# Kernel tuning notes

Hardware: AMD Instinct MI355X
Metric: run time of the kernel (lower is better)

## Reference

```python
import jax, jax.numpy as jnp
import numpy as np

NUM_HEADS = 32
NUM_KV_HEADS = 8
HEAD_DIM = 128
ROPE_THETA = 10000.0


def rotate_half(x):
    x1, x2 = jnp.split(x, 2, axis=-1)
    return jnp.concatenate((-x2, x1), axis=-1)


def setup_inputs() -> dict:
    key = jax.random.key(0)
    ks = jax.random.split(key, 5)
    B, S, H = 1, 2048, 4096
    KV = NUM_KV_HEADS * HEAD_DIM
    return {
        "hidden_states": jax.random.normal(ks[0], (B, S, H), dtype=jnp.float32),
        "position_ids": jnp.arange(S, dtype=jnp.int64 if jax.config.jax_enable_x64 else jnp.int32)[None, :].repeat(B, axis=0),
        "Wq": jax.random.normal(ks[1], (H, H), dtype=jnp.float32) * 0.02,
        "Wk": jax.random.normal(ks[2], (KV, H), dtype=jnp.float32) * 0.02,
        "Wv": jax.random.normal(ks[3], (KV, H), dtype=jnp.float32) * 0.02,
        "Wo": jax.random.normal(ks[4], (H, H), dtype=jnp.float32) * 0.02,
    }


def reference(hidden_states, position_ids, Wq, Wk, Wv, Wo):
    B, S, H = hidden_states.shape
    nh, nkv, hd = NUM_HEADS, NUM_KV_HEADS, HEAD_DIM
    n_rep = nh // nkv

    # QKV projections (torch Linear: y = x @ W^T)
    q = jnp.einsum('bsh,oh->bso', hidden_states, Wq).reshape(B, S, nh, hd).transpose(0, 2, 1, 3)
    k = jnp.einsum('bsh,oh->bso', hidden_states, Wk).reshape(B, S, nkv, hd).transpose(0, 2, 1, 3)
    v = jnp.einsum('bsh,oh->bso', hidden_states, Wv).reshape(B, S, nkv, hd).transpose(0, 2, 1, 3)

    # RoPE: cos/sin [B, 1, S, hd]
    inv_freq = 1.0 / (ROPE_THETA ** (jnp.arange(0, hd, 2, dtype=jnp.float32) / hd))
    freqs = position_ids.astype(jnp.float32)[..., None] * inv_freq  # [B, S, hd/2]
    emb = jnp.concatenate((freqs, freqs), axis=-1)                  # [B, S, hd]
    cos = jnp.cos(emb)[:, None, :, :]
    sin = jnp.sin(emb)[:, None, :, :]
    q = q * cos + rotate_half(q) * sin
    k = k * cos + rotate_half(k) * sin

    # GQA repeat_kv: [B, nkv, S, hd] -> [B, nh, S, hd]
    k = jnp.repeat(k, n_rep, axis=1)
    v = jnp.repeat(v, n_rep, axis=1)

    # eager attention with causal mask, softmax in fp32
    scores = jnp.einsum('bhqd,bhkd->bhqk', q, k) / jnp.sqrt(jnp.float32(hd))
    causal = jnp.tril(jnp.ones((S, S), dtype=bool))
    scores = jnp.where(causal[None, None], scores, jnp.finfo(scores.dtype).min)
    probs = jax.nn.softmax(scores.astype(jnp.float32), axis=-1).astype(q.dtype)
    attn = jnp.einsum('bhqk,bhkd->bhqd', probs, v)

    out = attn.transpose(0, 2, 1, 3).reshape(B, S, nh * hd)
    return jnp.einsum('bso,ho->bsh', out, Wo)
```

## Files before the change

kernel.cpp:

```cpp
#include <hip/hip_runtime.h>

typedef __bf16 bf16x8 __attribute__((ext_vector_type(8)));
typedef float f32x4 __attribute__((ext_vector_type(4)));
typedef unsigned int u32x4 __attribute__((ext_vector_type(4)));
typedef unsigned short u16x4 __attribute__((ext_vector_type(4)));
typedef unsigned short ushort_t;

#define S_LEN 2048
#define HDIM  4096
#define KVDIM 1024
#define NHEAD 32
#define NKV   8

__device__ __forceinline__ unsigned short f2b(float x) {
    unsigned int u = __builtin_bit_cast(unsigned int, x);
    u = (u + 0x7FFFu + ((u >> 16) & 1u)) >> 16;
    return (unsigned short)u;
}
__device__ __forceinline__ float b2f(unsigned short b) {
    unsigned int u = ((unsigned int)b) << 16;
    return __builtin_bit_cast(float, u);
}

__device__ __forceinline__ void gl_lds16(const void* g, void* s) {
    __builtin_amdgcn_global_load_lds(
        (const __attribute__((address_space(1))) unsigned int*)g,
        (__attribute__((address_space(3))) unsigned int*)s, 16, 0, 0);
}

__global__ void cvt_kernel(const float* __restrict__ in, unsigned short* __restrict__ out, int n4) {
    int i = blockIdx.x * 256 + threadIdx.x;
    if (i >= n4) return;
    f32x4 v = ((const f32x4*)in)[i];
    u16x4 o;
    o.x = f2b(v.x); o.y = f2b(v.y); o.z = f2b(v.z); o.w = f2b(v.w);
    ((u16x4*)out)[i] = o;
}

template <int MODE>
__device__ __forceinline__ void gemm_body(const unsigned short* __restrict__ A,
                                          const unsigned short* __restrict__ B,
                                          void* __restrict__ Cv,
                                          int M, int N, int K, int m0, int n0,
                                          unsigned short (*As)[64], unsigned short (*Bs)[64]) {
    const int tid = threadIdx.x;
    const int w = tid >> 6, lane = tid & 63, quad = lane >> 4, l15 = lane & 15;
    const int wy = w >> 1, wx = w & 1;
    const int srowb = w * 32 + (lane >> 3);
    const int gchunk = (lane & 7) ^ (lane >> 3);
    const int lcol = (lane & 7) * 8;

    f32x4 acc[4][4] = {};

    for (int k0 = 0; k0 < K; k0 += 64) {
#pragma unroll
        for (int p = 0; p < 4; ++p) {
            int r = srowb + p * 8;
            gl_lds16(&A[(size_t)(m0 + r) * K + k0 + gchunk * 8], &As[r][lcol]);
            gl_lds16(&B[(size_t)(n0 + r) * K + k0 + gchunk * 8], &Bs[r][lcol]);
        }
        __syncthreads();
#pragma unroll
        for (int t = 0; t < 2; ++t) {
            bf16x8 af[4], bfr[4];
#pragma unroll
            for (int mb = 0; mb < 4; ++mb)
                af[mb] = *(const bf16x8*)&As[wy * 64 + mb * 16 + l15][(((t * 4 + quad) ^ (l15 & 7)) * 8)];
#pragma unroll
            for (int nb = 0; nb < 4; ++nb)
                bfr[nb] = *(const bf16x8*)&Bs[wx * 64 + nb * 16 + l15][(((t * 4 + quad) ^ (l15 & 7)) * 8)];
#pragma unroll
            for (int mb = 0; mb < 4; ++mb)
#pragma unroll
                for (int nb = 0; nb < 4; ++nb)
                    acc[mb][nb] = __builtin_amdgcn_mfma_f32_16x16x32_bf16(af[mb], bfr[nb], acc[mb][nb], 0, 0, 0);
        }
        __syncthreads();
    }
#pragma unroll
    for (int mb = 0; mb < 4; ++mb)
#pragma unroll
        for (int nb = 0; nb < 4; ++nb)
#pragma unroll
            for (int r = 0; r < 4; ++r) {
                int row = m0 + wy * 64 + mb * 16 + quad * 4 + r;
                int col = n0 + wx * 64 + nb * 16 + l15;
                float v = acc[mb][nb][r];
                if (MODE == 0)
                    ((unsigned short*)Cv)[(size_t)row * N + col] = f2b(v);
                else if (MODE == 1)
                    ((unsigned short*)Cv)[(size_t)col * M + row] = f2b(v);
                else
                    ((float*)Cv)[(size_t)row * N + col] = v;
            }
}

template <int MODE>
__global__ __launch_bounds__(256) void gemm_nt(const unsigned short* __restrict__ A,
                                               const unsigned short* __restrict__ B,
                                               void* __restrict__ Cv, int M, int N, int K) {
    __shared__ unsigned short As[128][64];
    __shared__ unsigned short Bs[128][64];
    gemm_body<MODE>(A, B, Cv, M, N, K, blockIdx.y * 128, blockIdx.x * 128, As, Bs);
}

__global__ __launch_bounds__(256) void gemm_kv(const unsigned short* __restrict__ A,
                                               const unsigned short* __restrict__ Bk,
                                               const unsigned short* __restrict__ Bv,
                                               void* __restrict__ Ck, void* __restrict__ Cvt,
                                               int M, int K) {
    __shared__ unsigned short As[128][64];
    __shared__ unsigned short Bs[128][64];
    if (blockIdx.x < 8)
        gemm_body<0>(A, Bk, Ck, M, KVDIM, K, blockIdx.y * 128, blockIdx.x * 128, As, Bs);
    else
        gemm_body<1>(A, Bv, Cvt, M, KVDIM, K, blockIdx.y * 128, (blockIdx.x - 8) * 128, As, Bs);
}

__global__ void rope_kernel(unsigned short* __restrict__ Q, unsigned short* __restrict__ Kc,
                            const int* __restrict__ pos_ids) {
    int tid = blockIdx.x * 256 + threadIdx.x;
    int j = tid & 63;
    int head = (tid >> 6) % (NHEAD + NKV);
    int s = tid / (64 * (NHEAD + NKV));
    float pos = (float)pos_ids[s];
    float inv = exp2f(-(float)j * 0.20762050593046f);
    float ang = pos * inv;
    float sn, cs;
    __sincosf(ang, &sn, &cs);
    unsigned short* p;
    if (head < NHEAD)
        p = Q + (size_t)s * HDIM + head * 128;
    else
        p = Kc + (size_t)s * KVDIM + (head - NHEAD) * 128;
    float x1 = b2f(p[j]), x2 = b2f(p[j + 64]);
    p[j] = f2b(x1 * cs - x2 * sn);
    p[j + 64] = f2b(x2 * cs + x1 * sn);
}

__global__ __launch_bounds__(256) void attn_fwd(const unsigned short* __restrict__ Q,
                                                const unsigned short* __restrict__ Kb,
                                                const unsigned short* __restrict__ Vt,
                                                unsigned short* __restrict__ O) {
    __shared__ unsigned short Ks[64][136];
    __shared__ unsigned short Vts[128][72];
    __shared__ unsigned short Ps[4][16][80];

    const int qblk = (gridDim.y - 1) - blockIdx.y;
    const int h = blockIdx.x, kvh = h >> 2;
    const int tid = threadIdx.x, w = tid >> 6, lane = tid & 63;
    const int quad = lane >> 4, l15 = lane & 15;
    const int qg = qblk * 64 + w * 16 + l15;

    bf16x8 aq[4];
#pragma unroll
    for (int t = 0; t < 4; ++t)
        aq[t] = *(const bf16x8*)&Q[(size_t)qg * HDIM + h * 128 + t * 32 + quad * 8];

    f32x4 o[8] = {};
    float m_s = -3.0e38f, l_s = 0.f;
    const float cexp = 0.08838834764831845f * 1.4426950408889634f;

    const int kr0 = tid >> 4, ksg = tid & 15;
    const int vr0 = tid >> 3, vsg = tid & 7;

    u32x4 kpre[4], vpre[4];
#pragma unroll
    for (int p = 0; p < 4; ++p) {
        kpre[p] = *(const u32x4*)&Kb[(size_t)(kr0 + p * 16) * KVDIM + kvh * 128 + ksg * 8];
        vpre[p] = *(const u32x4*)&Vt[(size_t)(kvh * 128 + vr0 + p * 32) * S_LEN + vsg * 8];
    }

    for (int kt = 0; kt <= qblk; ++kt) {
#pragma unroll
        for (int p = 0; p < 4; ++p) {
            *(u32x4*)&Ks[kr0 + p * 16][ksg * 8] = kpre[p];
            *(u32x4*)&Vts[vr0 + p * 32][vsg * 8] = vpre[p];
        }
        __syncthreads();
        if (kt < qblk) {
            const int k0n = kt * 64 + 64;
#pragma unroll
            for (int p = 0; p < 4; ++p) {
                kpre[p] = *(const u32x4*)&Kb[(size_t)(k0n + kr0 + p * 16) * KVDIM + kvh * 128 + ksg * 8];
                vpre[p] = *(const u32x4*)&Vt[(size_t)(kvh * 128 + vr0 + p * 32) * S_LEN + k0n + vsg * 8];
            }
        }

        f32x4 sc[4] = {};
#pragma unroll
        for (int t = 0; t < 4; ++t)
#pragma unroll
            for (int mb = 0; mb < 4; ++mb) {
                bf16x8 ak = *(const bf16x8*)&Ks[mb * 16 + l15][t * 32 + quad * 8];
                sc[mb] = __builtin_amdgcn_mfma_f32_16x16x32_bf16(ak, aq[t], sc[mb], 0, 0, 0);
            }

        float vv[16];
        if (kt == qblk) {
#pragma unroll
            for (int mb = 0; mb < 4; ++mb)
#pragma unroll
                for (int r = 0; r < 4; ++r) {
                    int kl = mb * 16 + quad * 4 + r;
                    vv[mb * 4 + r] = (kl <= w * 16 + l15) ? sc[mb][r] * cexp : -3.0e38f;
                }
        } else {
#pragma unroll
            for (int mb = 0; mb < 4; ++mb)
#pragma unroll
                for (int r = 0; r < 4; ++r)
                    vv[mb * 4 + r] = sc[mb][r] * cexp;
        }
        float mx = vv[0];
#pragma unroll
        for (int i = 1; i < 16; ++i) mx = fmaxf(mx, vv[i]);
        mx = fmaxf(mx, __shfl_xor(mx, 16, 64));
        mx = fmaxf(mx, __shfl_xor(mx, 32, 64));
        float mnew = fmaxf(m_s, mx);
        float alpha = exp2f(m_s - mnew);
        m_s = mnew;
        float sum = 0.f;
        unsigned short pb[16];
#pragma unroll
        for (int i = 0; i < 16; ++i) {
            float pp = exp2f(vv[i] - mnew);
            sum += pp;
            pb[i] = f2b(pp);
        }
        sum += __shfl_xor(sum, 16, 64);
        sum += __shfl_xor(sum, 32, 64);
        l_s = l_s * alpha + sum;
#pragma unroll
        for (int mb = 0; mb < 4; ++mb) {
            u16x4 pk = {pb[mb * 4 + 0], pb[mb * 4 + 1], pb[mb * 4 + 2], pb[mb * 4 + 3]};
            *(u16x4*)&Ps[w][l15][mb * 16 + quad * 4] = pk;
        }
        float a4[4];
#pragma unroll
        for (int r = 0; r < 4; ++r) a4[r] = __shfl(alpha, quad * 20 + r, 64);
#pragma unroll
        for (int db = 0; db < 8; ++db)
#pragma unroll
            for (int r = 0; r < 4; ++r) o[db][r] *= a4[r];

        bf16x8 pa[2];
#pragma unroll
        for (int t = 0; t < 2; ++t)
            pa[t] = *(const bf16x8*)&Ps[w][l15][t * 32 + quad * 8];
#pragma unroll
        for (int db = 0; db < 8; ++db)
#pragma unroll
            for (int t = 0; t < 2; ++t) {
                bf16x8 vb = *(const bf16x8*)&Vts[db * 16 + l15][t * 32 + quad * 8];
                o[db] = __builtin_amdgcn_mfma_f32_16x16x32_bf16(pa[t], vb, o[db], 0, 0, 0);
            }
        __syncthreads();
    }

    float linv[4];
#pragma unroll
    for (int r = 0; r < 4; ++r) linv[r] = 1.0f / __shfl(l_s, quad * 20 + r, 64);
    const int qrow_base = qblk * 64 + w * 16 + quad * 4;
#pragma unroll
    for (int db = 0; db < 8; ++db)
#pragma unroll
        for (int r = 0; r < 4; ++r) {
            int row = qrow_base + r;
            int col = h * 128 + db * 16 + l15;
            O[(size_t)row * HDIM + col] = f2b(o[db][r] * linv[r]);
        }
}

extern "C" void kernel_launch(void* const* d_in, const int* in_sizes, int n_in,
                              void* d_out, int out_size, void* d_ws, size_t ws_size,
                              hipStream_t stream) {
    const float* hid = (const float*)d_in[0];
    const int* pos   = (const int*)d_in[1];
    const float* Wq  = (const float*)d_in[2];
    const float* Wk  = (const float*)d_in[3];
    const float* Wv  = (const float*)d_in[4];
    const float* Wo  = (const float*)d_in[5];
    float* out = (float*)d_out;

    char* ws = (char*)d_ws;
    unsigned short* hb   = (unsigned short*)(ws);
    unsigned short* Wqb  = (unsigned short*)(ws + 16777216);
    unsigned short* Wkb  = (unsigned short*)(ws + 50331648);
    unsigned short* Wvb  = (unsigned short*)(ws + 58720256);
    unsigned short* Wob  = (unsigned short*)(ws + 67108864);
    unsigned short* Qw   = (unsigned short*)(ws + 100663296);
    unsigned short* Kw   = (unsigned short*)(ws + 117440512);
    unsigned short* Vtw  = Wqb;
    unsigned short* attw = hb;

    cvt_kernel<<<(S_LEN * HDIM / 4 + 255) / 256, 256, 0, stream>>>(hid, hb, S_LEN * HDIM / 4);
    cvt_kernel<<<(HDIM * HDIM / 4 + 255) / 256, 256, 0, stream>>>(Wq, Wqb, HDIM * HDIM / 4);
    cvt_kernel<<<(KVDIM * HDIM / 4 + 255) / 256, 256, 0, stream>>>(Wk, Wkb, KVDIM * HDIM / 4);
    cvt_kernel<<<(KVDIM * HDIM / 4 + 255) / 256, 256, 0, stream>>>(Wv, Wvb, KVDIM * HDIM / 4);
    cvt_kernel<<<(HDIM * HDIM / 4 + 255) / 256, 256, 0, stream>>>(Wo, Wob, HDIM * HDIM / 4);

    gemm_nt<0><<<dim3(HDIM / 128, S_LEN / 128), 256, 0, stream>>>(hb, Wqb, Qw, S_LEN, HDIM, HDIM);
    gemm_kv<<<dim3(16, S_LEN / 128), 256, 0, stream>>>(hb, Wkb, Wvb, Kw, Vtw, S_LEN, HDIM);

    rope_kernel<<<S_LEN * (NHEAD + NKV) * 64 / 256, 256, 0, stream>>>(Qw, Kw, pos);

    attn_fwd<<<dim3(NHEAD, S_LEN / 64), 256, 0, stream>>>(Qw, Kw, Vtw, attw);

    gemm_nt<2><<<dim3(HDIM / 128, S_LEN / 128), 256, 0, stream>>>(attw, Wob, out, S_LEN, HDIM, HDIM);
}
```

Measured before the change: 561.0 us.

## Merge conversions and QKV GEMMs, use 128-row attention tiles with swizzled LDS

The five fp32-to-bf16 conversion launches become one kernel, and the Q and KV projection GEMMs become a single launch with 48 column blocks. V-transpose moves to its own workspace slot so it no longer aliases Wqb. The attention kernel now processes 128 query rows per block, two 16-row sub-tiles per wave, which halves K/V reloads across query blocks. It also drops LDS padding in favour of an XOR swizzle, skips fully masked sub-tiles, and sets a three-blocks-per-CU occupancy hint. These changes target launch overhead, K/V memory traffic and LDS bank conflicts, but raise register pressure and halve the number of attention blocks.

```diff
diff --git a/kernel.cpp b/kernel.cpp
--- a/kernel.cpp
+++ b/kernel.cpp
@@ -4,7 +4,6 @@
 typedef float f32x4 __attribute__((ext_vector_type(4)));
 typedef unsigned int u32x4 __attribute__((ext_vector_type(4)));
 typedef unsigned short u16x4 __attribute__((ext_vector_type(4)));
-typedef unsigned short ushort_t;
 
 #define S_LEN 2048
 #define HDIM  4096
@@ -28,13 +27,23 @@
         (__attribute__((address_space(3))) unsigned int*)s, 16, 0, 0);
 }
 
-__global__ void cvt_kernel(const float* __restrict__ in, unsigned short* __restrict__ out, int n4) {
-    int i = blockIdx.x * 256 + threadIdx.x;
-    if (i >= n4) return;
-    f32x4 v = ((const f32x4*)in)[i];
+__global__ void cvt_all(const float* __restrict__ hid, const float* __restrict__ Wq,
+                        const float* __restrict__ Wk, const float* __restrict__ Wv,
+                        const float* __restrict__ Wo,
+                        unsigned short* __restrict__ hb, unsigned short* __restrict__ Wqb,
+                        unsigned short* __restrict__ Wkb, unsigned short* __restrict__ Wvb,
+                        unsigned short* __restrict__ Wob) {
+    int g = blockIdx.x * 256 + threadIdx.x;
+    const float* src; unsigned short* dst; int off;
+    if (g < 2097152)      { src = hid; dst = hb;  off = g; }
+    else if (g < 6291456) { src = Wq;  dst = Wqb; off = g - 2097152; }
+    else if (g < 7340032) { src = Wk;  dst = Wkb; off = g - 6291456; }
+    else if (g < 8388608) { src = Wv;  dst = Wvb; off = g - 7340032; }
+    else                  { src = Wo;  dst = Wob; off = g - 8388608; }
+    f32x4 v = ((const f32x4*)src)[off];
     u16x4 o;
     o.x = f2b(v.x); o.y = f2b(v.y); o.z = f2b(v.z); o.w = f2b(v.w);
-    ((u16x4*)out)[i] = o;
+    ((u16x4*)dst)[off] = o;
 }
 
 template <int MODE>
@@ -95,26 +104,29 @@
             }
 }
 
-template <int MODE>
-__global__ __launch_bounds__(256) void gemm_nt(const unsigned short* __restrict__ A,
-                                               const unsigned short* __restrict__ B,
-                                               void* __restrict__ Cv, int M, int N, int K) {
+__global__ __launch_bounds__(256) void gemm_qkv(const unsigned short* __restrict__ A,
+                                                const unsigned short* __restrict__ Bq,
+                                                const unsigned short* __restrict__ Bk,
+                                                const unsigned short* __restrict__ Bv,
+                                                void* __restrict__ Cq, void* __restrict__ Ck,
+                                                void* __restrict__ Cvt) {
     __shared__ unsigned short As[128][64];
     __shared__ unsigned short Bs[128][64];
-    gemm_body<MODE>(A, B, Cv, M, N, K, blockIdx.y * 128, blockIdx.x * 128, As, Bs);
-}
-
-__global__ __launch_bounds__(256) void gemm_kv(const unsigned short* __restrict__ A,
-                                               const unsigned short* __restrict__ Bk,
-                                               const unsigned short* __restrict__ Bv,
-                                               void* __restrict__ Ck, void* __restrict__ Cvt,
-                                               int M, int K) {
+    const int bx = blockIdx.x, m0 = blockIdx.y * 128;
+    if (bx < 32)
+        gemm_body<0>(A, Bq, Cq, S_LEN, HDIM, HDIM, m0, bx * 128, As, Bs);
+    else if (bx < 40)
+        gemm_body<0>(A, Bk, Ck, S_LEN, KVDIM, HDIM, m0, (bx - 32) * 128, As, Bs);
+    else
+        gemm_body<1>(A, Bv, Cvt, S_LEN, KVDIM, HDIM, m0, (bx - 40) * 128, As, Bs);
+}
+
+__global__ __launch_bounds__(256) void gemm_o(const unsigned short* __restrict__ A,
+                                              const unsigned short* __restrict__ B,
+                                              void* __restrict__ Cv) {
     __shared__ unsigned short As[128][64];
     __shared__ unsigned short Bs[128][64];
-    if (blockIdx.x < 8)
-        gemm_body<0>(A, Bk, Ck, M, KVDIM, K, blockIdx.y * 128, blockIdx.x * 128, As, Bs);
-    else
-        gemm_body<1>(A, Bv, Cvt, M, KVDIM, K, blockIdx.y * 128, (blockIdx.x - 8) * 128, As, Bs);
+    gemm_body<2>(A, B, Cv, S_LEN, HDIM, HDIM, blockIdx.y * 128, blockIdx.x * 128, As, Bs);
 }
 
 __global__ void rope_kernel(unsigned short* __restrict__ Q, unsigned short* __restrict__ Kc,
@@ -138,31 +150,34 @@
     p[j + 64] = f2b(x2 * cs + x1 * sn);
 }
 
-__global__ __launch_bounds__(256) void attn_fwd(const unsigned short* __restrict__ Q,
-                                                const unsigned short* __restrict__ Kb,
-                                                const unsigned short* __restrict__ Vt,
-                                                unsigned short* __restrict__ O) {
-    __shared__ unsigned short Ks[64][136];
-    __shared__ unsigned short Vts[128][72];
-    __shared__ unsigned short Ps[4][16][80];
-
-    const int qblk = (gridDim.y - 1) - blockIdx.y;
+__global__ __launch_bounds__(256, 3) void attn_fwd(const unsigned short* __restrict__ Q,
+                                                   const unsigned short* __restrict__ Kb,
+                                                   const unsigned short* __restrict__ Vt,
+                                                   unsigned short* __restrict__ O) {
+    __shared__ unsigned short Ks[64][128];
+    __shared__ unsigned short Vts[128][64];
+    __shared__ unsigned short Ps[4][2][16][80];
+
+    const int qb = (gridDim.y - 1) - blockIdx.y;
     const int h = blockIdx.x, kvh = h >> 2;
     const int tid = threadIdx.x, w = tid >> 6, lane = tid & 63;
     const int quad = lane >> 4, l15 = lane & 15;
-    const int qg = qblk * 64 + w * 16 + l15;
-
-    bf16x8 aq[4];
-#pragma unroll
-    for (int t = 0; t < 4; ++t)
-        aq[t] = *(const bf16x8*)&Q[(size_t)qg * HDIM + h * 128 + t * 32 + quad * 8];
-
-    f32x4 o[8] = {};
-    float m_s = -3.0e38f, l_s = 0.f;
+
+    bf16x8 aq[2][4];
+#pragma unroll
+    for (int u = 0; u < 2; ++u)
+#pragma unroll
+        for (int t = 0; t < 4; ++t)
+            aq[u][t] = *(const bf16x8*)&Q[(size_t)(qb * 128 + w * 32 + u * 16 + l15) * HDIM +
+                                          h * 128 + t * 32 + quad * 8];
+
+    f32x4 o[2][8] = {};
+    float m_s[2] = {-3.0e38f, -3.0e38f}, l_s[2] = {0.f, 0.f};
     const float cexp = 0.08838834764831845f * 1.4426950408889634f;
 
     const int kr0 = tid >> 4, ksg = tid & 15;
     const int vr0 = tid >> 3, vsg = tid & 7;
+    const int ktmax = 2 * qb + 1;
 
     u32x4 kpre[4], vpre[4];
 #pragma unroll
@@ -171,14 +186,16 @@
         vpre[p] = *(const u32x4*)&Vt[(size_t)(kvh * 128 + vr0 + p * 32) * S_LEN + vsg * 8];
     }
 
-    for (int kt = 0; kt <= qblk; ++kt) {
+    for (int kt = 0; kt <= ktmax; ++kt) {
 #pragma unroll
         for (int p = 0; p < 4; ++p) {
-            *(u32x4*)&Ks[kr0 + p * 16][ksg * 8] = kpre[p];
-            *(u32x4*)&Vts[vr0 + p * 32][vsg * 8] = vpre[p];
+            int rk = kr0 + p * 16;
+            *(u32x4*)&Ks[rk][(ksg ^ (rk & 7)) * 8] = kpre[p];
+            int rv = vr0 + p * 32;
+            *(u32x4*)&Vts[rv][(vsg ^ (rv & 7)) * 8] = vpre[p];
         }
         __syncthreads();
-        if (kt < qblk) {
+        if (kt < ktmax) {
             const int k0n = kt * 64 + 64;
 #pragma unroll
             for (int p = 0; p < 4; ++p) {
@@ -187,89 +204,91 @@
             }
         }
 
-        f32x4 sc[4] = {};
-#pragma unroll
-        for (int t = 0; t < 4; ++t)
+        const int k0 = kt * 64;
+#pragma unroll
+        for (int u = 0; u < 2; ++u) {
+            const int qmin = qb * 128 + w * 32 + u * 16;
+            if (k0 > qmin + 15) continue;
+
+            f32x4 sc[4] = {};
+#pragma unroll
+            for (int t = 0; t < 4; ++t)
+#pragma unroll
+                for (int mb = 0; mb < 4; ++mb) {
+                    bf16x8 ak = *(const bf16x8*)&Ks[mb * 16 + l15][((t * 4 + quad) ^ (l15 & 7)) * 8];
+                    sc[mb] = __builtin_amdgcn_mfma_f32_16x16x32_bf16(ak, aq[u][t], sc[mb], 0, 0, 0);
+                }
+
+            const bool need_mask = (k0 + 63 > qmin);
+            const int qg = qmin + l15;
+            float mx = -3.0e38f;
+#pragma unroll
+            for (int mb = 0; mb < 4; ++mb)
+#pragma unroll
+                for (int r = 0; r < 4; ++r) {
+                    float v = sc[mb][r] * cexp;
+                    if (need_mask && (k0 + mb * 16 + quad * 4 + r > qg)) v = -3.0e38f;
+                    mx = fmaxf(mx, v);
+                }
+            mx = fmaxf(mx, __shfl_xor(mx, 16, 64));
+            mx = fmaxf(mx, __shfl_xor(mx, 32, 64));
+            float mnew = fmaxf(m_s[u], mx);
+            float alpha = exp2f(m_s[u] - mnew);
+            m_s[u] = mnew;
+            float sum = 0.f;
 #pragma unroll
             for (int mb = 0; mb < 4; ++mb) {
-                bf16x8 ak = *(const bf16x8*)&Ks[mb * 16 + l15][t * 32 + quad * 8];
-                sc[mb] = __builtin_amdgcn_mfma_f32_16x16x32_bf16(ak, aq[t], sc[mb], 0, 0, 0);
+                u16x4 pk;
+#pragma unroll
+                for (int r = 0; r < 4; ++r) {
+                    float v = sc[mb][r] * cexp;
+                    float pp = (need_mask && (k0 + mb * 16 + quad * 4 + r > qg))
+                                   ? 0.f : exp2f(v - mnew);
+                    sum += pp;
+                    ((unsigned short*)&pk)[r] = f2b(pp);
+                }
+                *(u16x4*)&Ps[w][u][l15][mb * 16 + quad * 4] = pk;
             }
-
-        float vv[16];
-        if (kt == qblk) {
-#pragma unroll
-            for (int mb = 0; mb < 4; ++mb)
-#pragma unroll
-                for (int r = 0; r < 4; ++r) {
-                    int kl = mb * 16 + quad * 4 + r;
-                    vv[mb * 4 + r] = (kl <= w * 16 + l15) ? sc[mb][r] * cexp : -3.0e38f;
+            sum += __shfl_xor(sum, 16, 64);
+            sum += __shfl_xor(sum, 32, 64);
+            l_s[u] = l_s[u] * alpha + sum;
+
+            float a4[4];
+#pragma unroll
+            for (int r = 0; r < 4; ++r) a4[r] = __shfl(alpha, quad * 20 + r, 64);
+#pragma unroll
+            for (int db = 0; db < 8; ++db)
+#pragma unroll
+                for (int r = 0; r < 4; ++r) o[u][db][r] *= a4[r];
+
+            bf16x8 pa[2];
+#pragma unroll
+            for (int t = 0; t < 2; ++t)
+                pa[t] = *(const bf16x8*)&Ps[w][u][l15][t * 32 + quad * 8];
+#pragma unroll
+            for (int db = 0; db < 8; ++db)
+#pragma unroll
+                for (int t = 0; t < 2; ++t) {
+                    bf16x8 vb = *(const bf16x8*)&Vts[db * 16 + l15][((t * 4 + quad) ^ (l15 & 7)) * 8];
+                    o[u][db] = __builtin_amdgcn_mfma_f32_16x16x32_bf16(pa[t], vb, o[u][db], 0, 0, 0);
                 }
-        } else {
-#pragma unroll
-            for (int mb = 0; mb < 4; ++mb)
-#pragma unroll
-                for (int r = 0; r < 4; ++r)
-                    vv[mb * 4 + r] = sc[mb][r] * cexp;
-        }
-        float mx = vv[0];
-#pragma unroll
-        for (int i = 1; i < 16; ++i) mx = fmaxf(mx, vv[i]);
-        mx = fmaxf(mx, __shfl_xor(mx, 16, 64));
-        mx = fmaxf(mx, __shfl_xor(mx, 32, 64));
-        float mnew = fmaxf(m_s, mx);
-        float alpha = exp2f(m_s - mnew);
-        m_s = mnew;
-        float sum = 0.f;
-        unsigned short pb[16];
-#pragma unroll
-        for (int i = 0; i < 16; ++i) {
-            float pp = exp2f(vv[i] - mnew);
-            sum += pp;
-            pb[i] = f2b(pp);
-        }
-        sum += __shfl_xor(sum, 16, 64);
-        sum += __shfl_xor(sum, 32, 64);
-        l_s = l_s * alpha + sum;
-#pragma unroll
-        for (int mb = 0; mb < 4; ++mb) {
-            u16x4 pk = {pb[mb * 4 + 0], pb[mb * 4 + 1], pb[mb * 4 + 2], pb[mb * 4 + 3]};
-            *(u16x4*)&Ps[w][l15][mb * 16 + quad * 4] = pk;
-        }
-        float a4[4];
-#pragma unroll
-        for (int r = 0; r < 4; ++r) a4[r] = __shfl(alpha, quad * 20 + r, 64);
-#pragma unroll
-        for (int db = 0; db < 8; ++db)
-#pragma unroll
-            for (int r = 0; r < 4; ++r) o[db][r] *= a4[r];
-
-        bf16x8 pa[2];
-#pragma unroll
-        for (int t = 0; t < 2; ++t)
-            pa[t] = *(const bf16x8*)&Ps[w][l15][t * 32 + quad * 8];
-#pragma unroll
-        for (int db = 0; db < 8; ++db)
-#pragma unroll
-            for (int t = 0; t < 2; ++t) {
-                bf16x8 vb = *(const bf16x8*)&Vts[db * 16 + l15][t * 32 + quad * 8];
-                o[db] = __builtin_amdgcn_mfma_f32_16x16x32_bf16(pa[t], vb, o[db], 0, 0, 0);
-            }
+        }
         __syncthreads();
     }
 
-    float linv[4];
-#pragma unroll
-    for (int r = 0; r < 4; ++r) linv[r] = 1.0f / __shfl(l_s, quad * 20 + r, 64);
-    const int qrow_base = qblk * 64 + w * 16 + quad * 4;
-#pragma unroll
-    for (int db = 0; db < 8; ++db)
-#pragma unroll
-        for (int r = 0; r < 4; ++r) {
-            int row = qrow_base + r;
-            int col = h * 128 + db * 16 + l15;
-            O[(size_t)row * HDIM + col] = f2b(o[db][r] * linv[r]);
-        }
+#pragma unroll
+    for (int u = 0; u < 2; ++u) {
+        float linv[4];
+#pragma unroll
+        for (int r = 0; r < 4; ++r) linv[r] = 1.0f / __shfl(l_s[u], quad * 20 + r, 64);
+        const int qrow_base = qb * 128 + w * 32 + u * 16 + quad * 4;
+#pragma unroll
+        for (int db = 0; db < 8; ++db)
+#pragma unroll
+            for (int r = 0; r < 4; ++r)
+                O[(size_t)(qrow_base + r) * HDIM + h * 128 + db * 16 + l15] =
+                    f2b(o[u][db][r] * linv[r]);
+    }
 }
 
 extern "C" void kernel_launch(void* const* d_in, const int* in_sizes, int n_in,
@@ -291,21 +310,16 @@
     unsigned short* Wob  = (unsigned short*)(ws + 67108864);
     unsigned short* Qw   = (unsigned short*)(ws + 100663296);
     unsigned short* Kw   = (unsigned short*)(ws + 117440512);
-    unsigned short* Vtw  = Wqb;
+    unsigned short* Vtw  = (unsigned short*)(ws + 121634816);
     unsigned short* attw = hb;
 
-    cvt_kernel<<<(S_LEN * HDIM / 4 + 255) / 256, 256, 0, stream>>>(hid, hb, S_LEN * HDIM / 4);
-    cvt_kernel<<<(HDIM * HDIM / 4 + 255) / 256, 256, 0, stream>>>(Wq, Wqb, HDIM * HDIM / 4);
-    cvt_kernel<<<(KVDIM * HDIM / 4 + 255) / 256, 256, 0, stream>>>(Wk, Wkb, KVDIM * HDIM / 4);
-    cvt_kernel<<<(KVDIM * HDIM / 4 + 255) / 256, 256, 0, stream>>>(Wv, Wvb, KVDIM * HDIM / 4);
-    cvt_kernel<<<(HDIM * HDIM / 4 + 255) / 256, 256, 0, stream>>>(Wo, Wob, HDIM * HDIM / 4);
-
-    gemm_nt<0><<<dim3(HDIM / 128, S_LEN / 128), 256, 0, stream>>>(hb, Wqb, Qw, S_LEN, HDIM, HDIM);
-    gemm_kv<<<dim3(16, S_LEN / 128), 256, 0, stream>>>(hb, Wkb, Wvb, Kw, Vtw, S_LEN, HDIM);
+    cvt_all<<<49152, 256, 0, stream>>>(hid, Wq, Wk, Wv, Wo, hb, Wqb, Wkb, Wvb, Wob);
+
+    gemm_qkv<<<dim3(48, S_LEN / 128), 256, 0, stream>>>(hb, Wqb, Wkb, Wvb, Qw, Kw, Vtw);
 
     rope_kernel<<<S_LEN * (NHEAD + NKV) * 64 / 256, 256, 0, stream>>>(Qw, Kw, pos);
 
-    attn_fwd<<<dim3(NHEAD, S_LEN / 64), 256, 0, stream>>>(Qw, Kw, Vtw, attw);
-
-    gemm_nt<2><<<dim3(HDIM / 128, S_LEN / 128), 256, 0, stream>>>(attw, Wob, out, S_LEN, HDIM, HDIM);
-}
+    attn_fwd<<<dim3(NHEAD, S_LEN / 128), 256, 0, stream>>>(Qw, Kw, Vtw, attw);
+
+    gemm_o<<<dim3(HDIM / 128, S_LEN / 128), 256, 0, stream>>>(attw, Wob, out);
+}
```

After: 721.8 us. 28.7% more time.
